# Kernel tuning notes

Measured on AMD Instinct MI355X. Metric: run time of the kernel, lower is better.

The kernel has to match this reference:

```python
import jax, jax.numpy as jnp
import numpy as np

L = 2   # number of classes (labels are 0/1 per docstring)
S = 4   # number of sessions
LAMBDA_CENTER = 1.0
LAMBDA_ALIGN = 1.0
EPS = 1e-8  # matches torch F.cosine_similarity default eps


def _cos(a, b):
    # cosine similarity along last dim, torch-style eps clamping of norms
    na = jnp.maximum(jnp.linalg.norm(a, axis=-1), EPS)
    nb = jnp.maximum(jnp.linalg.norm(b, axis=-1), EPS)
    return jnp.sum(a * b, axis=-1) / (na * nb)


def setup_inputs() -> dict:
    key = jax.random.key(0)
    k1, k2, k3 = jax.random.split(key, 3)
    B, D = 1048576, 128
    features = jax.random.normal(k1, (B, D), dtype=jnp.float32)
    labels = jax.random.randint(k2, (B,), 0, L, dtype=jnp.int32)
    sessions = jax.random.randint(k3, (B,), 0, S, dtype=jnp.int32)
    return {"features": features, "labels": labels, "sessions": sessions}


def reference(features, labels, sessions):
    B, D = features.shape
    gid = labels * S + sessions                       # (B,) group id in [0, L*S)
    sums = jax.ops.segment_sum(features, gid, num_segments=L * S)     # (L*S, D)
    counts = jax.ops.segment_sum(jnp.ones((B,), features.dtype), gid,
                                 num_segments=L * S)                  # (L*S,)
    centers = sums / counts[:, None]                  # per-(label,session) mean

    # center loss: mean over samples of (1 - cos(feat_i, center of its group))
    c_i = centers[gid]                                # (B, D) gather
    center_loss = jnp.mean(1.0 - _cos(features, c_i))

    # align loss: per class, pull session centers toward class prototype.
    # Faithfully replicates the original running-division: after each class y
    # the accumulated loss is divided by the number of that class's centers.
    centers_ls = centers.reshape(L, S, D)
    proto = centers_ls.mean(axis=1)                   # (L, D)
    per_class = jnp.sum(1.0 - _cos(centers_ls, proto[:, None, :]), axis=1)  # (L,)
    align_loss = jnp.zeros((), features.dtype)
    for y in range(L):
        align_loss = (align_loss + per_class[y]) / S

    total = LAMBDA_CENTER * center_loss + LAMBDA_ALIGN * align_loss
    return total, center_loss, align_loss
```

## Files before the change

kernel.cpp:

```cpp
#include <hip/hip_runtime.h>
#include <hip/hip_bf16.h>

#define NGROUPS 8
#define DIM 128
#define WS_FLOATS 2056
#define NBLK 2048
#define F_OFFSET ((size_t)NBLK * WS_FLOATS)

typedef float f32x4 __attribute__((ext_vector_type(4)));

template <int CTRL>
__device__ __forceinline__ float dpp_add(float x) {
    int s = __builtin_amdgcn_update_dpp(0, __float_as_int(x), CTRL, 0xF, 0xF, true);
    return x + __int_as_float(s);
}

__device__ __forceinline__ float2 pair_rnorm(float ss) {
    float r = ss;
    r = dpp_add<0x111>(r);
    r = dpp_add<0x112>(r);
    r = dpp_add<0x114>(r);
    r = dpp_add<0x118>(r);
    r = dpp_add<0x142>(r);
    float inv = fminf(__builtin_amdgcn_rsqf(r), 1e8f);
    float a = __int_as_float(__builtin_amdgcn_readlane(__float_as_int(inv), 31));
    float b = __int_as_float(__builtin_amdgcn_readlane(__float_as_int(inv), 63));
    return make_float2(a, b);
}

#define PAIRLOAD(V, M)                                                   \
    {                                                                    \
        int r1_ = __ffsll((long long)(M)) - 1; (M) &= (M) - 1;           \
        bool h2_ = ((M) != 0ull);                                        \
        int r2_ = r1_;                                                   \
        if (h2_) { r2_ = __ffsll((long long)(M)) - 1; (M) &= (M) - 1; }  \
        int row_ = (lane < 32) ? r1_ : r2_;                              \
        V = feat4[(size_t)(span + row_) * 32 + sub];                     \
        if (!h2_ && lane >= 32) V = zzz;                                 \
    }

#define PAIRPROC(V)                                                      \
    {                                                                    \
        float ss_ = (V).x * (V).x + (V).y * (V).y                        \
                  + (V).z * (V).z + (V).w * (V).w;                       \
        float2 rr_ = pair_rnorm(ss_);                                    \
        float rn_ = (lane < 32) ? rr_.x : rr_.y;                         \
        sa0 += (V).x; sa1 += (V).y; sa2 += (V).z; sa3 += (V).w;          \
        wa0 = fmaf(rn_, (V).x, wa0); wa1 = fmaf(rn_, (V).y, wa1);        \
        wa2 = fmaf(rn_, (V).z, wa2); wa3 = fmaf(rn_, (V).w, wa3);        \
    }

__global__ __launch_bounds__(256, 8)
void csca_accum_kernel(const f32x4* __restrict__ feat4,
                       const int* __restrict__ labels,
                       const int* __restrict__ sessions,
                       float* __restrict__ gws, int B) {
    __shared__ float s_all[WS_FLOATS];
    for (int i = threadIdx.x; i < WS_FLOATS; i += 256) s_all[i] = 0.0f;
    __syncthreads();

    const int lane = threadIdx.x & 63;
    const int sub = lane & 31;
    const int wid = __builtin_amdgcn_readfirstlane(blockIdx.x * 4 + (threadIdx.x >> 6));
    const int q = wid & 7;
    const int oct = wid >> 3;
    const int NOCT = (gridDim.x * 4) >> 3;
    const int step = NOCT * 64;
    const f32x4 zzz = {0.0f, 0.0f, 0.0f, 0.0f};

    float sa0 = 0.0f, sa1 = 0.0f, sa2 = 0.0f, sa3 = 0.0f;
    float wa0 = 0.0f, wa1 = 0.0f, wa2 = 0.0f, wa3 = 0.0f;
    int cntq = 0;

    int span0 = oct * 64;
    if (span0 + 63 < B) {
        int lb = labels[span0 + lane];
        int se = sessions[span0 + lane];

        for (int span = span0; span + 63 < B; span += step) {
            const int nspan = span + step;
            int nlb = 0, nse = 0;
            if (nspan + 63 < B) {
                nlb = labels[nspan + lane];
                nse = sessions[nspan + lane];
            }

            const int g = lb * 4 + se;
            unsigned long long m = __ballot(g == q);
            cntq += (int)__popcll(m);

            if (m != 0ull) {
                f32x4 va, vb;
                PAIRLOAD(va, m);
                while (m != 0ull) {
                    PAIRLOAD(vb, m);
                    PAIRPROC(va);
                    va = vb;
                }
                PAIRPROC(va);
            }

            lb = nlb; se = nse;
        }
    }

    sa0 += __shfl_xor(sa0, 32); sa1 += __shfl_xor(sa1, 32);
    sa2 += __shfl_xor(sa2, 32); sa3 += __shfl_xor(sa3, 32);
    wa0 += __shfl_xor(wa0, 32); wa1 += __shfl_xor(wa1, 32);
    wa2 += __shfl_xor(wa2, 32); wa3 += __shfl_xor(wa3, 32);

    if (lane < 32) {
        s_all[q * DIM + 4 * lane]     = sa0;
        s_all[q * DIM + 4 * lane + 1] = sa1;
        s_all[q * DIM + 4 * lane + 2] = sa2;
        s_all[q * DIM + 4 * lane + 3] = sa3;
        s_all[1024 + q * DIM + 4 * lane]     = wa0;
        s_all[1024 + q * DIM + 4 * lane + 1] = wa1;
        s_all[1024 + q * DIM + 4 * lane + 2] = wa2;
        s_all[1024 + q * DIM + 4 * lane + 3] = wa3;
    }
    if (lane == 0) s_all[2048 + q] = (float)cntq;
    __syncthreads();

    float* myP = gws + (size_t)blockIdx.x * WS_FLOATS;
    for (int i = threadIdx.x; i < WS_FLOATS; i += 256) myP[i] = s_all[i];
}

__global__ __launch_bounds__(256)
void csca_reduce_kernel(const float* __restrict__ gws, float* __restrict__ F) {
    const int i = blockIdx.x * 256 + threadIdx.x;
    if (i >= WS_FLOATS) return;
    const int r0 = blockIdx.y * (NBLK / 32);
    float s = 0.0f;
#pragma unroll 8
    for (int k = 0; k < NBLK / 32; ++k)
        s += gws[(size_t)(r0 + k) * WS_FLOATS + i];
    atomicAdd(&F[i], s);
}

__global__ __launch_bounds__(256)
void csca_finalize_kernel(const float* __restrict__ F, float* __restrict__ out, float invB) {
    __shared__ float red[WS_FLOATS];
    for (int i = threadIdx.x; i < WS_FLOATS; i += 256) red[i] = F[i];
    __syncthreads();

    if (threadIdx.x < 64) {
        const int lane = threadIdx.x;
        const float* sums  = red;
        const float* wsums = red + 1024;
        const float* cnts  = red + 2048;
        __shared__ float c_lds[NGROUPS][DIM];
        float cnorm2[NGROUPS];
        float cos_sum = 0.0f;

#pragma unroll
        for (int g = 0; g < NGROUPS; ++g) {
            float invc = 1.0f / cnts[g];
            float c0 = sums[g * DIM + lane] * invc;
            float c1 = sums[g * DIM + 64 + lane] * invc;
            c_lds[g][lane] = c0;
            c_lds[g][64 + lane] = c1;
            float w0 = wsums[g * DIM + lane];
            float w1 = wsums[g * DIM + 64 + lane];
            float pcc = c0 * c0 + c1 * c1;
            float pwc = w0 * c0 + w1 * c1;
#pragma unroll
            for (int m = 1; m < 64; m <<= 1) {
                pcc += __shfl_xor(pcc, m);
                pwc += __shfl_xor(pwc, m);
            }
            cnorm2[g] = pcc;
            cos_sum += pwc / fmaxf(sqrtf(pcc), 1e-8f);
        }
        float center_loss = 1.0f - cos_sum * invB;

        float align = 0.0f;
#pragma unroll
        for (int y = 0; y < 2; ++y) {
            float p0 = 0.0f, p1 = 0.0f;
#pragma unroll
            for (int s = 0; s < 4; ++s) {
                p0 += c_lds[4 * y + s][lane];
                p1 += c_lds[4 * y + s][64 + lane];
            }
            p0 *= 0.25f; p1 *= 0.25f;
            float ppp = p0 * p0 + p1 * p1;
#pragma unroll
            for (int m = 1; m < 64; m <<= 1) ppp += __shfl_xor(ppp, m);
            float pn = fmaxf(sqrtf(ppp), 1e-8f);
            float pc = 0.0f;
#pragma unroll
            for (int s = 0; s < 4; ++s) {
                float d = c_lds[4 * y + s][lane] * p0 + c_lds[4 * y + s][64 + lane] * p1;
#pragma unroll
                for (int m = 1; m < 64; m <<= 1) d += __shfl_xor(d, m);
                float cs = d / (fmaxf(sqrtf(cnorm2[4 * y + s]), 1e-8f) * pn);
                pc += 1.0f - cs;
            }
            align = (align + pc) * 0.25f;
        }

        if (lane == 0) {
            out[0] = center_loss + align;
            out[1] = center_loss;
            out[2] = align;
        }
    }
}

extern "C" void kernel_launch(void* const* d_in, const int* in_sizes, int n_in,
                              void* d_out, int out_size, void* d_ws, size_t ws_size,
                              hipStream_t stream) {
    const float* feat = (const float*)d_in[0];
    const int* labels = (const int*)d_in[1];
    const int* sessions = (const int*)d_in[2];
    const int B = in_sizes[1];
    float* gws = (float*)d_ws;
    float* F = gws + F_OFFSET;

    hipMemsetAsync(F, 0, WS_FLOATS * sizeof(float), stream);

    csca_accum_kernel<<<NBLK, 256, 0, stream>>>((const f32x4*)feat, labels, sessions, gws, B);
    csca_reduce_kernel<<<dim3(9, 32), 256, 0, stream>>>(gws, F);
    csca_finalize_kernel<<<1, 256, 0, stream>>>(F, (float*)d_out, 1.0f / (float)B);
}
```

Before: 120.9 us.

## Replace per-block partials and reduce kernel with direct global atomics

Each wave now adds its per-group sums, weighted sums and counts straight into the final global accumulator with float atomics. This removes the shared-memory staging, the large per-block workspace write and the separate reduction kernel launch. In exchange it adds heavy atomic contention on about 2K addresses and makes the summation order non-deterministic.

```diff
diff --git a/kernel.cpp b/kernel.cpp
--- a/kernel.cpp
+++ b/kernel.cpp
@@ -5,7 +5,6 @@
 #define DIM 128
 #define WS_FLOATS 2056
 #define NBLK 2048
-#define F_OFFSET ((size_t)NBLK * WS_FLOATS)
 
 typedef float f32x4 __attribute__((ext_vector_type(4)));
 
@@ -54,11 +53,7 @@
 void csca_accum_kernel(const f32x4* __restrict__ feat4,
                        const int* __restrict__ labels,
                        const int* __restrict__ sessions,
-                       float* __restrict__ gws, int B) {
-    __shared__ float s_all[WS_FLOATS];
-    for (int i = threadIdx.x; i < WS_FLOATS; i += 256) s_all[i] = 0.0f;
-    __syncthreads();
-
+                       float* __restrict__ F, int B) {
     const int lane = threadIdx.x & 63;
     const int sub = lane & 31;
     const int wid = __builtin_amdgcn_readfirstlane(blockIdx.x * 4 + (threadIdx.x >> 6));
@@ -110,32 +105,14 @@
     wa2 += __shfl_xor(wa2, 32); wa3 += __shfl_xor(wa3, 32);
 
     if (lane < 32) {
-        s_all[q * DIM + 4 * lane]     = sa0;
-        s_all[q * DIM + 4 * lane + 1] = sa1;
-        s_all[q * DIM + 4 * lane + 2] = sa2;
-        s_all[q * DIM + 4 * lane + 3] = sa3;
-        s_all[1024 + q * DIM + 4 * lane]     = wa0;
-        s_all[1024 + q * DIM + 4 * lane + 1] = wa1;
-        s_all[1024 + q * DIM + 4 * lane + 2] = wa2;
-        s_all[1024 + q * DIM + 4 * lane + 3] = wa3;
-    }
-    if (lane == 0) s_all[2048 + q] = (float)cntq;
-    __syncthreads();
-
-    float* myP = gws + (size_t)blockIdx.x * WS_FLOATS;
-    for (int i = threadIdx.x; i < WS_FLOATS; i += 256) myP[i] = s_all[i];
-}
-
-__global__ __launch_bounds__(256)
-void csca_reduce_kernel(const float* __restrict__ gws, float* __restrict__ F) {
-    const int i = blockIdx.x * 256 + threadIdx.x;
-    if (i >= WS_FLOATS) return;
-    const int r0 = blockIdx.y * (NBLK / 32);
-    float s = 0.0f;
-#pragma unroll 8
-    for (int k = 0; k < NBLK / 32; ++k)
-        s += gws[(size_t)(r0 + k) * WS_FLOATS + i];
-    atomicAdd(&F[i], s);
+        float* Fs = F + q * DIM + 4 * lane;
+        atomicAdd(Fs + 0, sa0); atomicAdd(Fs + 1, sa1);
+        atomicAdd(Fs + 2, sa2); atomicAdd(Fs + 3, sa3);
+        float* Fw = F + 1024 + q * DIM + 4 * lane;
+        atomicAdd(Fw + 0, wa0); atomicAdd(Fw + 1, wa1);
+        atomicAdd(Fw + 2, wa2); atomicAdd(Fw + 3, wa3);
+    }
+    if (lane == 0) atomicAdd(&F[2048 + q], (float)cntq);
 }
 
 __global__ __launch_bounds__(256)
@@ -215,12 +192,10 @@
     const int* labels = (const int*)d_in[1];
     const int* sessions = (const int*)d_in[2];
     const int B = in_sizes[1];
-    float* gws = (float*)d_ws;
-    float* F = gws + F_OFFSET;
+    float* F = (float*)d_ws;
 
     hipMemsetAsync(F, 0, WS_FLOATS * sizeof(float), stream);
 
-    csca_accum_kernel<<<NBLK, 256, 0, stream>>>((const f32x4*)feat, labels, sessions, gws, B);
-    csca_reduce_kernel<<<dim3(9, 32), 256, 0, stream>>>(gws, F);
+    csca_accum_kernel<<<NBLK, 256, 0, stream>>>((const f32x4*)feat, labels, sessions, F, B);
     csca_finalize_kernel<<<1, 256, 0, stream>>>(F, (float*)d_out, 1.0f / (float)B);
 }
```

Result: slower. 195.0 us (+61.3%).
